# Performance work log

Hardware: AMD Instinct MI355X
Metric: run time of the kernel (lower is better)

The kernel has to match this reference:

```python
import jax, jax.numpy as jnp
import numpy as np

B, D, C, H, L = 32768, 64, 64, 1024, 6
EPS = 1e-5
NIN = (D - D // 2) + C  # unchanged half + cond = 96
SPLIT = D // 2          # 32


def setup_inputs() -> dict:
    key = jax.random.key(0)
    ks = jax.random.split(key, 12)
    s = 0.05
    return {
        "z": jax.random.normal(ks[0], (B, D), jnp.float32),
        "cond": jax.random.normal(ks[1], (B, C), jnp.float32),
        "W1": jax.random.normal(ks[2], (L, NIN, H), jnp.float32) * s,
        "b1": jax.random.normal(ks[3], (L, H), jnp.float32) * s,
        "W2": jax.random.normal(ks[4], (L, H, H), jnp.float32) * s,
        "b2": jax.random.normal(ks[5], (L, H), jnp.float32) * s,
        "Ws": jax.random.normal(ks[6], (L, H, SPLIT), jnp.float32) * s,
        "bs": jax.random.normal(ks[7], (L, SPLIT), jnp.float32) * s,
        "Wt": jax.random.normal(ks[8], (L, H, SPLIT), jnp.float32) * s,
        "bt": jax.random.normal(ks[9], (L, SPLIT), jnp.float32) * s,
        "bn_w": 1.0 + 0.1 * jax.random.normal(ks[10], (L, D), jnp.float32),
        "bn_b": 0.1 * jax.random.normal(ks[11], (L, D), jnp.float32),
    }


def reference(z, cond, W1, b1, W2, b2, Ws, bs, Wt, bt, bn_w, bn_b):
    x = z
    log_det = jnp.zeros((z.shape[0],), z.dtype)
    for i in range(L):
        # 'even' mask keeps even indices on even layers, odd indices otherwise
        if i % 2 == 0:
            keep, chg = np.arange(0, D, 2), np.arange(1, D, 2)
        else:
            keep, chg = np.arange(1, D, 2), np.arange(0, D, 2)
        # 2-layer MLP on [x_keep, cond]
        h = jax.nn.relu(jnp.concatenate([x[:, keep], cond], axis=1) @ W1[i] + b1[i])
        h = jax.nn.relu(h @ W2[i] + b2[i])
        log_s = jnp.tanh(h @ Ws[i] + bs[i])          # (B, SPLIT)
        t = h @ Wt[i] + bt[i]                         # (B, SPLIT)
        x2t = x[:, chg] * jnp.exp(log_s) + t
        x = jnp.zeros_like(x).at[:, keep].set(x[:, keep]).at[:, chg].set(x2t)
        log_det = log_det + log_s.sum(axis=1)
        # BatchNorm1d, training mode: batch mean / biased variance, eps=1e-5
        mean = x.mean(axis=0)
        var = x.var(axis=0)
        x = (x - mean) * jax.lax.rsqrt(var + EPS) * bn_w[i] + bn_b[i]
        log_det = log_det + jnp.log(jnp.abs(bn_w[i])).sum()
    return x, log_det
```

## Files before the change

kernel.cpp:

```cpp
#include <hip/hip_runtime.h>
#include <math.h>

#define BB 32768
#define DD 64
#define CC 64
#define HH 1024
#define LL 6
#define SPLIT 32
#define NIN 96
#define EPSV 1e-5f

typedef short short8 __attribute__((ext_vector_type(8)));
typedef float f32x4 __attribute__((ext_vector_type(4)));
typedef unsigned short u16;

__device__ __forceinline__ u16 f2bf(float f) {
    union { float f; unsigned int u; } c; c.f = f;
    unsigned int u = c.u + 0x7FFFu + ((c.u >> 16) & 1u);
    return (u16)(u >> 16);
}

__device__ __forceinline__ void gl_lds16(const u16* g, u16* l) {
    __builtin_amdgcn_global_load_lds(
        (const __attribute__((address_space(1))) unsigned int*)g,
        (__attribute__((address_space(3))) unsigned int*)l, 16, 0, 0);
}

#define DSR(dst, addr, off) \
    asm volatile("ds_read_b128 %0, %1 offset:" #off : "=&v"(dst) : "v"(addr))

__global__ void transpose_cvt_kernel(const float* __restrict__ src, u16* __restrict__ dst,
                                     int R, int C, int Rpad,
                                     long long sstride, long long dstride)
{
    __shared__ float tile[32][33];
    const float* s = src + (size_t)blockIdx.z * sstride;
    u16* d = dst + (size_t)blockIdx.z * dstride;
    int r0 = blockIdx.x * 32, c0 = blockIdx.y * 32;
    int tc = threadIdx.x & 31, tr = threadIdx.x >> 5;
#pragma unroll
    for (int i = 0; i < 4; ++i) {
        int r = r0 + tr + i * 8;
        tile[tr + i * 8][tc] = (r < R) ? s[(size_t)r * C + c0 + tc] : 0.f;
    }
    __syncthreads();
#pragma unroll
    for (int i = 0; i < 4; ++i) {
        int cc = tr + i * 8;
        d[(size_t)(c0 + cc) * Rpad + r0 + tc] = f2bf(tile[tc][cc]);
    }
}

__global__ __launch_bounds__(256)
void init_ain_cond_kernel(const float* __restrict__ cond, u16* __restrict__ Ain)
{
    int t = blockIdx.x * 256 + threadIdx.x;
    int c = t % 96, r = t / 96;
    Ain[(size_t)r * 128 + 32 + c] = (c < CC) ? f2bf(cond[(size_t)r * CC + c]) : (u16)0;
}

__global__ __launch_bounds__(256)
void build_keep_kernel(const float* __restrict__ x, u16* __restrict__ Ain, int keep_off)
{
    int t = blockIdx.x * 256 + threadIdx.x;
    int c = t & 31, r = t >> 5;
    Ain[(size_t)r * 128 + c] = f2bf(x[(size_t)r * DD + 2 * c + keep_off]);
}

__global__ __launch_bounds__(512, 2)
void gemm_tiled(const u16* __restrict__ A,
                const u16* __restrict__ Bt,
                const float* __restrict__ bias,
                u16* __restrict__ Cc,
                int K)
{
    __shared__ u16 sA[2][32 * 512];
    __shared__ u16 sB[2][32 * 512];

    const int t = threadIdx.x;
    const int w = t >> 6, lane = t & 63;
    const int lane16 = lane & 15, quad = lane >> 4;
    const int wm = w >> 2, wn = w & 3;

    int id = blockIdx.x;
    int nby = gridDim.x >> 2;
    int xcd = id & 7, slot = id >> 3;
    int bx = slot & 3, byq = slot >> 2;
    int by = xcd * (nby >> 3) + byq;
    const int bm = by * 256, bn = bx * 256;

    const int ntile = K >> 6;

    auto stage_half = [&](int kt, int op, int s, int buf) {
        int k0 = kt * 64 + s * 32 + quad * 8;
#pragma unroll
        for (int r = 0; r < 2; ++r) {
            int i = r * 8 + w;
            int e = s * 16 + i;
            if (op == 0) {
                const u16* g = A + (size_t)(bm + i * 16 + lane16) * K + k0;
                gl_lds16(g, &sA[buf][e * 512]);
            } else {
                const u16* g = Bt + (size_t)(bn + i * 16 + lane16) * K + k0;
                gl_lds16(g, &sB[buf][e * 512]);
            }
        }
    };

    f32x4 acc[8][4];
#pragma unroll
    for (int a = 0; a < 8; ++a)
#pragma unroll
        for (int b = 0; b < 4; ++b) acc[a][b] = (f32x4){0.f, 0.f, 0.f, 0.f};

    const unsigned sAb = (unsigned)(size_t)(__attribute__((address_space(3))) u16*)&sA[0][0];
    const unsigned sBb = (unsigned)(size_t)(__attribute__((address_space(3))) u16*)&sB[0][0];
    const unsigned aoff = (unsigned)(wm * 8 * 1024 + lane * 16);
    const unsigned boff = (unsigned)(wn * 4 * 1024 + lane * 16);

    stage_half(0, 0, 0, 0);
    stage_half(0, 1, 0, 0);
    stage_half(0, 0, 1, 0);
    stage_half(0, 1, 1, 0);
    asm volatile("s_waitcnt vmcnt(0)");
    __builtin_amdgcn_s_barrier();

    short8 af[4], ag[4], bf[4], bg[4];
    for (int kt = 0; kt < ntile; ++kt) {
        const unsigned base = (unsigned)((kt & 1) << 15);
        const unsigned aA0 = sAb + base + aoff;
        const unsigned aB0 = sBb + base + boff;
        const unsigned aA1 = aA0 + 16384;
        const unsigned aB1 = aB0 + 16384;
        const int nb = (kt + 1) & 1;
        const bool more = (kt + 1 < ntile);

        DSR(bf[0], aB0, 0); DSR(bf[1], aB0, 1024);
        DSR(bf[2], aB0, 2048); DSR(bf[3], aB0, 3072);
        DSR(af[0], aA0, 0); DSR(af[1], aA0, 1024);
        DSR(af[2], aA0, 2048); DSR(af[3], aA0, 3072);
        if (more) { stage_half(kt + 1, 0, 0, nb); stage_half(kt + 1, 1, 0, nb); }
        DSR(ag[0], aA0, 4096); DSR(ag[1], aA0, 5120);
        DSR(ag[2], aA0, 6144); DSR(ag[3], aA0, 7168);
        asm volatile("s_waitcnt lgkmcnt(4)");
        __builtin_amdgcn_sched_barrier(0);
        __builtin_amdgcn_s_setprio(1);
#pragma unroll
        for (int a = 0; a < 4; ++a)
#pragma unroll
            for (int b = 0; b < 4; ++b)
                acc[a][b] = __builtin_amdgcn_mfma_f32_16x16x32_bf16(af[a], bf[b], acc[a][b], 0, 0, 0);
        __builtin_amdgcn_s_setprio(0);

        if (more) { stage_half(kt + 1, 0, 1, nb); stage_half(kt + 1, 1, 1, nb); }
        DSR(bg[0], aB1, 0); DSR(bg[1], aB1, 1024);
        DSR(bg[2], aB1, 2048); DSR(bg[3], aB1, 3072);
        DSR(af[0], aA1, 0); DSR(af[1], aA1, 1024);
        DSR(af[2], aA1, 2048); DSR(af[3], aA1, 3072);
        asm volatile("s_waitcnt lgkmcnt(8)");
        __builtin_amdgcn_sched_barrier(0);
        __builtin_amdgcn_s_setprio(1);
#pragma unroll
        for (int a = 0; a < 4; ++a)
#pragma unroll
            for (int b = 0; b < 4; ++b)
                acc[4 + a][b] = __builtin_amdgcn_mfma_f32_16x16x32_bf16(ag[a], bf[b], acc[4 + a][b], 0, 0, 0);
        __builtin_amdgcn_s_setprio(0);

        DSR(ag[0], aA1, 4096); DSR(ag[1], aA1, 5120);
        DSR(ag[2], aA1, 6144); DSR(ag[3], aA1, 7168);
        asm volatile("s_waitcnt lgkmcnt(4)");
        __builtin_amdgcn_sched_barrier(0);
        __builtin_amdgcn_s_setprio(1);
#pragma unroll
        for (int a = 0; a < 4; ++a)
#pragma unroll
            for (int b = 0; b < 4; ++b)
                acc[a][b] = __builtin_amdgcn_mfma_f32_16x16x32_bf16(af[a], bg[b], acc[a][b], 0, 0, 0);
        __builtin_amdgcn_s_setprio(0);

        asm volatile("s_waitcnt lgkmcnt(0)");
        __builtin_amdgcn_sched_barrier(0);
        __builtin_amdgcn_s_setprio(1);
#pragma unroll
        for (int a = 0; a < 4; ++a)
#pragma unroll
            for (int b = 0; b < 4; ++b)
                acc[4 + a][b] = __builtin_amdgcn_mfma_f32_16x16x32_bf16(ag[a], bg[b], acc[4 + a][b], 0, 0, 0);
        __builtin_amdgcn_s_setprio(0);

        asm volatile("s_waitcnt vmcnt(0)");
        __builtin_amdgcn_s_barrier();
    }
    __syncthreads();

    constexpr int ES = 72;
    float bv[4];
#pragma unroll
    for (int b = 0; b < 4; ++b) bv[b] = bias[bn + wn * 64 + b * 16 + lane16];
    u16* scr = ((u16*)sB) + w * (16 * ES);
#pragma unroll
    for (int a = 0; a < 8; ++a) {
#pragma unroll
        for (int b = 0; b < 4; ++b)
#pragma unroll
            for (int r = 0; r < 4; ++r) {
                float v = fmaxf(acc[a][b][r] + bv[b], 0.f);
                scr[(quad * 4 + r) * ES + b * 16 + lane16] = f2bf(v);
            }
#pragma unroll
        for (int ch = 0; ch < 2; ++ch) {
            int row = ch * 8 + (lane >> 3), colc = (lane & 7) * 8;
            short8 v = *(const short8*)(scr + row * ES + colc);
            *(short8*)(Cc + (size_t)(bm + wm * 128 + a * 16 + row) * 1024 + bn + wn * 64 + colc) = v;
        }
    }
}

__global__ __launch_bounds__(512, 2)
void gemm1_once(const u16* __restrict__ A,
                const u16* __restrict__ Bt,
                const float* __restrict__ bias,
                u16* __restrict__ Cc)
{
    __shared__ u16 sA[2][32 * 512];
    __shared__ u16 sB[2][32 * 512];

    const int t = threadIdx.x;
    const int w = t >> 6, lane = t & 63;
    const int lane16 = lane & 15, quad = lane >> 4;
    const int wm = w >> 2, wn = w & 3;

    int id = blockIdx.x;
    int nby = gridDim.x >> 2;
    int xcd = id & 7, slot = id >> 3;
    int bx = slot & 3, byq = slot >> 2;
    int by = xcd * (nby >> 3) + byq;
    const int bm = by * 256, bn = bx * 256;

    auto stage_half = [&](int kt, int op, int s, int buf) {
        int k0 = kt * 64 + s * 32 + quad * 8;
#pragma unroll
        for (int r = 0; r < 2; ++r) {
            int i = r * 8 + w;
            int e = s * 16 + i;
            if (op == 0) {
                const u16* g = A + (size_t)(bm + i * 16 + lane16) * 128 + k0;
                gl_lds16(g, &sA[buf][e * 512]);
            } else {
                const u16* g = Bt + (size_t)(bn + i * 16 + lane16) * 128 + k0;
                gl_lds16(g, &sB[buf][e * 512]);
            }
        }
    };

    f32x4 acc[8][4];
#pragma unroll
    for (int a = 0; a < 8; ++a)
#pragma unroll
        for (int b = 0; b < 4; ++b) acc[a][b] = (f32x4){0.f, 0.f, 0.f, 0.f};

    const unsigned sAb = (unsigned)(size_t)(__attribute__((address_space(3))) u16*)&sA[0][0];
    const unsigned sBb = (unsigned)(size_t)(__attribute__((address_space(3))) u16*)&sB[0][0];
    const unsigned aoff = (unsigned)(wm * 8 * 1024 + lane * 16);
    const unsigned boff = (unsigned)(wn * 4 * 1024 + lane * 16);

#pragma unroll
    for (int kt = 0; kt < 2; ++kt) {
        stage_half(kt, 0, 0, kt);
        stage_half(kt, 1, 0, kt);
        stage_half(kt, 0, 1, kt);
        stage_half(kt, 1, 1, kt);
    }
    __syncthreads();

    short8 af[4], ag[4], bf[4], bg[4];
#pragma unroll
    for (int kt = 0; kt < 2; ++kt) {
        const unsigned base = (unsigned)(kt << 15);
        const unsigned aA0 = sAb + base + aoff;
        const unsigned aB0 = sBb + base + boff;
        const unsigned aA1 = aA0 + 16384;
        const unsigned aB1 = aB0 + 16384;

        DSR(bf[0], aB0, 0); DSR(bf[1], aB0, 1024);
        DSR(bf[2], aB0, 2048); DSR(bf[3], aB0, 3072);
        DSR(af[0], aA0, 0); DSR(af[1], aA0, 1024);
        DSR(af[2], aA0, 2048); DSR(af[3], aA0, 3072);
        DSR(ag[0], aA0, 4096); DSR(ag[1], aA0, 5120);
        DSR(ag[2], aA0, 6144); DSR(ag[3], aA0, 7168);
        asm volatile("s_waitcnt lgkmcnt(4)");
        __builtin_amdgcn_sched_barrier(0);
        __builtin_amdgcn_s_setprio(1);
#pragma unroll
        for (int a = 0; a < 4; ++a)
#pragma unroll
            for (int b = 0; b < 4; ++b)
                acc[a][b] = __builtin_amdgcn_mfma_f32_16x16x32_bf16(af[a], bf[b], acc[a][b], 0, 0, 0);
        __builtin_amdgcn_s_setprio(0);

        DSR(bg[0], aB1, 0); DSR(bg[1], aB1, 1024);
        DSR(bg[2], aB1, 2048); DSR(bg[3], aB1, 3072);
        DSR(af[0], aA1, 0); DSR(af[1], aA1, 1024);
        DSR(af[2], aA1, 2048); DSR(af[3], aA1, 3072);
        asm volatile("s_waitcnt lgkmcnt(8)");
        __builtin_amdgcn_sched_barrier(0);
        __builtin_amdgcn_s_setprio(1);
#pragma unroll
        for (int a = 0; a < 4; ++a)
#pragma unroll
            for (int b = 0; b < 4; ++b)
                acc[4 + a][b] = __builtin_amdgcn_mfma_f32_16x16x32_bf16(ag[a], bf[b], acc[4 + a][b], 0, 0, 0);
        __builtin_amdgcn_s_setprio(0);

        DSR(ag[0], aA1, 4096); DSR(ag[1], aA1, 5120);
        DSR(ag[2], aA1, 6144); DSR(ag[3], aA1, 7168);
        asm volatile("s_waitcnt lgkmcnt(4)");
        __builtin_amdgcn_sched_barrier(0);
        __builtin_amdgcn_s_setprio(1);
#pragma unroll
        for (int a = 0; a < 4; ++a)
#pragma unroll
            for (int b = 0; b < 4; ++b)
                acc[a][b] = __builtin_amdgcn_mfma_f32_16x16x32_bf16(af[a], bg[b], acc[a][b], 0, 0, 0);
        __builtin_amdgcn_s_setprio(0);

        asm volatile("s_waitcnt lgkmcnt(0)");
        __builtin_amdgcn_sched_barrier(0);
        __builtin_amdgcn_s_setprio(1);
#pragma unroll
        for (int a = 0; a < 4; ++a)
#pragma unroll
            for (int b = 0; b < 4; ++b)
                acc[4 + a][b] = __builtin_amdgcn_mfma_f32_16x16x32_bf16(ag[a], bg[b], acc[4 + a][b], 0, 0, 0);
        __builtin_amdgcn_s_setprio(0);
    }
    __syncthreads();

    constexpr int ES = 72;
    float bv[4];
#pragma unroll
    for (int b = 0; b < 4; ++b) bv[b] = bias[bn + wn * 64 + b * 16 + lane16];
    u16* scr = ((u16*)sB) + w * (16 * ES);
#pragma unroll
    for (int a = 0; a < 8; ++a) {
#pragma unroll
        for (int b = 0; b < 4; ++b)
#pragma unroll
            for (int r = 0; r < 4; ++r) {
                float v = fmaxf(acc[a][b][r] + bv[b], 0.f);
                scr[(quad * 4 + r) * ES + b * 16 + lane16] = f2bf(v);
            }
#pragma unroll
        for (int ch = 0; ch < 2; ++ch) {
            int row = ch * 8 + (lane >> 3), colc = (lane & 7) * 8;
            short8 v = *(const short8*)(scr + row * ES + colc);
            *(short8*)(Cc + (size_t)(bm + wm * 128 + a * 16 + row) * 1024 + bn + wn * 64 + colc) = v;
        }
    }
}

__global__ __launch_bounds__(512)
void gemm3_coupling(const u16* __restrict__ A,
                    const u16* __restrict__ Bt,
                    const float* __restrict__ bs, const float* __restrict__ bt,
                    float* __restrict__ x, float* __restrict__ log_det,
                    float* __restrict__ stat_sum, float* __restrict__ stat_sumsq,
                    int keep_off, int row0)
{
    constexpr int ST_STRIDE = 66;
    __shared__ u16 sB[128 * 512];
    __shared__ float ssum[8][64], ssum2[8][64];
    float* sst = (float*)sB;

    const int t = threadIdx.x;
    const int w = t >> 6, lane = t & 63;
    const int lane16 = lane & 15, quad = lane >> 4;
    const int bm = blockIdx.x * 128;

#pragma unroll
    for (int r = 0; r < 16; ++r) {
        int e = r * 8 + w;
        int s = e >> 2, j = e & 3;
        const u16* g = Bt + (size_t)(j * 16 + lane16) * HH + s * 32 + quad * 8;
        gl_lds16(g, &sB[e * 512]);
    }

    f32x4 acc[4];
#pragma unroll
    for (int j = 0; j < 4; ++j) acc[j] = (f32x4){0.f, 0.f, 0.f, 0.f};

    const u16* Arow = A + (size_t)(bm + w * 16 + lane16) * HH + quad * 8;

    __syncthreads();

#pragma unroll 4
    for (int s = 0; s < 32; ++s) {
        short8 af = *(const short8*)(Arow + s * 32);
        const u16* bb = sB + s * 2048 + lane * 8;
#pragma unroll
        for (int j = 0; j < 4; ++j) {
            short8 bfr = *(const short8*)(bb + j * 512);
            acc[j] = __builtin_amdgcn_mfma_f32_16x16x32_bf16(af, bfr, acc[j], 0, 0, 0);
        }
    }
    __syncthreads();

#pragma unroll
    for (int j = 0; j < 4; ++j)
#pragma unroll
        for (int r = 0; r < 4; ++r)
            sst[(w * 16 + quad * 4 + r) * ST_STRIDE + j * 16 + lane16] = acc[j][r];
    __syncthreads();

    const int f = lane;
    const bool is_chg = ((f & 1) != keep_off);
    const int j = f >> 1;
    float bsj = 0.f, btj = 0.f;
    if (is_chg) { bsj = bs[j]; btj = bt[j]; }

    float lsum = 0.f, lsum2 = 0.f;
    for (int i = 0; i < 16; ++i) {
        int crow = w * 16 + i;
        int grow = row0 + bm + crow;
        float xv = x[(size_t)grow * DD + f];
        float ld = 0.f;
        if (is_chg) {
            float s_raw = sst[crow * ST_STRIDE + j];
            float t_raw = sst[crow * ST_STRIDE + SPLIT + j];
            float ls = tanhf(s_raw + bsj);
            float tv = t_raw + btj;
            xv = xv * expf(ls) + tv;
            x[(size_t)grow * DD + f] = xv;
            ld = ls;
        }
        for (int off = 32; off > 0; off >>= 1) ld += __shfl_down(ld, off, 64);
        if (f == 0) log_det[grow] += ld;
        lsum  += xv;
        lsum2 += xv * xv;
    }

    ssum[w][f]  = lsum;
    ssum2[w][f] = lsum2;
    __syncthreads();
    if (t < 64) {
        float a = 0.f, b = 0.f;
#pragma unroll
        for (int g = 0; g < 8; ++g) { a += ssum[g][t]; b += ssum2[g][t]; }
        atomicAdd(stat_sum + t, a);
        atomicAdd(stat_sumsq + t, b);
    }
}

__global__ __launch_bounds__(256)
void normalize_kernel(const float* __restrict__ xin, float* __restrict__ xout,
                      const float* __restrict__ stat_sum, const float* __restrict__ stat_sumsq,
                      const float* __restrict__ bn_w, const float* __restrict__ bn_b,
                      float* __restrict__ log_det,
                      u16* __restrict__ Ain, int off_next)
{
    __shared__ float sscale[64], sshift[64], scsum;
    int t = threadIdx.x;
    if (t < 64) {
        const float invB = 1.f / (float)BB;
        float mean = stat_sum[t] * invB;
        float var  = stat_sumsq[t] * invB - mean * mean;
        float inv  = rsqrtf(var + EPSV);
        float wv   = bn_w[t];
        float sc   = inv * wv;
        sscale[t] = sc;
        sshift[t] = bn_b[t] - mean * sc;
        float lg = logf(fabsf(wv));
        for (int off = 32; off > 0; off >>= 1) lg += __shfl_down(lg, off, 64);
        if (t == 0) scsum = lg;
    }
    __syncthreads();

    int idx = blockIdx.x * blockDim.x + t;
    int f0 = (idx & 15) * 4;
    int row = idx >> 4;
    float4 v = ((const float4*)xin)[idx];
    v.x = v.x * sscale[f0 + 0] + sshift[f0 + 0];
    v.y = v.y * sscale[f0 + 1] + sshift[f0 + 1];
    v.z = v.z * sscale[f0 + 2] + sshift[f0 + 2];
    v.w = v.w * sscale[f0 + 3] + sshift[f0 + 3];
    ((float4*)xout)[idx] = v;
    if ((idx & 15) == 0) log_det[row] += scsum;
    if (Ain) {
        float a0 = off_next ? v.y : v.x;
        float a1 = off_next ? v.w : v.z;
        ushort2 u; u.x = f2bf(a0); u.y = f2bf(a1);
        *(ushort2*)(Ain + (size_t)row * 128 + (f0 >> 1)) = u;
    }
}

extern "C" void kernel_launch(void* const* d_in, const int* in_sizes, int n_in,
                              void* d_out, int out_size, void* d_ws, size_t ws_size,
                              hipStream_t stream)
{
    const float* z    = (const float*)d_in[0];
    const float* cond = (const float*)d_in[1];
    const float* W1   = (const float*)d_in[2];
    const float* b1   = (const float*)d_in[3];
    const float* W2   = (const float*)d_in[4];
    const float* b2   = (const float*)d_in[5];
    const float* Ws   = (const float*)d_in[6];
    const float* bs   = (const float*)d_in[7];
    const float* Wt   = (const float*)d_in[8];
    const float* bt   = (const float*)d_in[9];
    const float* bn_w = (const float*)d_in[10];
    const float* bn_b = (const float*)d_in[11];

    float* out_x  = (float*)d_out;
    float* out_ld = out_x + (size_t)BB * DD;

    char* p = (char*)d_ws;
    size_t used = 0;
    auto alloc = [&](size_t bytes) { void* q = p + used; used += (bytes + 255) & ~(size_t)255; return q; };

    float* xbuf = (float*)alloc((size_t)BB * DD * 4);
    u16*   w1t  = (u16*)alloc((size_t)LL * HH * 128 * 2);
    u16*   w2t  = (u16*)alloc((size_t)LL * HH * HH * 2);
    u16*   wstt = (u16*)alloc((size_t)LL * 64 * HH * 2);
    u16*   Ain  = (u16*)alloc((size_t)BB * 128 * 2);
    float* stat_sum   = (float*)alloc(64 * 4);
    float* stat_sumsq = (float*)alloc(64 * 4);

    int CH = BB;
    while (CH > 8192 && used + (size_t)CH * 4096 + 4096 > ws_size) CH >>= 1;
    u16* h1 = (u16*)alloc((size_t)CH * HH * 2);
    u16* h2 = (u16*)alloc((size_t)CH * HH * 2);

    hipMemcpyAsync(xbuf, z, (size_t)BB * DD * sizeof(float), hipMemcpyDeviceToDevice, stream);
    hipMemsetAsync(out_ld, 0, (size_t)BB * sizeof(float), stream);

    transpose_cvt_kernel<<<dim3(128/32, HH/32, LL), 256, 0, stream>>>(
        W1, w1t, NIN, HH, 128, (long long)NIN * HH, (long long)HH * 128);
    transpose_cvt_kernel<<<dim3(HH/32, HH/32, LL), 256, 0, stream>>>(
        W2, w2t, HH, HH, HH, (long long)HH * HH, (long long)HH * HH);
    transpose_cvt_kernel<<<dim3(HH/32, SPLIT/32, LL), 256, 0, stream>>>(
        Ws, wstt, HH, SPLIT, HH, (long long)HH * SPLIT, (long long)64 * HH);
    transpose_cvt_kernel<<<dim3(HH/32, SPLIT/32, LL), 256, 0, stream>>>(
        Wt, wstt + (size_t)SPLIT * HH, HH, SPLIT, HH, (long long)HH * SPLIT, (long long)64 * HH);

    init_ain_cond_kernel<<<BB * 96 / 256, 256, 0, stream>>>(cond, Ain);
    build_keep_kernel<<<BB * 32 / 256, 256, 0, stream>>>(xbuf, Ain, 0);

    for (int l = 0; l < LL; ++l) {
        const int off = l & 1;
        hipMemsetAsync(stat_sum, 0, 2 * 64 * sizeof(float), stream);

        for (int c = 0; c < BB / CH; ++c) {
            const int row0 = c * CH;

            gemm1_once<<<(CH / 256) * 4, 512, 0, stream>>>(
                Ain + (size_t)row0 * 128, w1t + (size_t)l * HH * 128,
                b1 + (size_t)l * HH, h1);

            gemm_tiled<<<(CH / 256) * 4, 512, 0, stream>>>(
                h1, w2t + (size_t)l * HH * HH,
                b2 + (size_t)l * HH, h2, HH);

            gemm3_coupling<<<CH / 128, 512, 0, stream>>>(
                h2, wstt + (size_t)l * 64 * HH,
                bs + (size_t)l * SPLIT, bt + (size_t)l * SPLIT,
                xbuf, out_ld, stat_sum, stat_sumsq, off, row0);
        }

        float* xout = (l == LL - 1) ? out_x : xbuf;
        u16* ain_next = (l < LL - 1) ? Ain : nullptr;
        normalize_kernel<<<(BB * DD / 4) / 256, 256, 0, stream>>>(
            xbuf, xout, stat_sum, stat_sumsq,
            bn_w + (size_t)l * DD, bn_b + (size_t)l * DD,
            out_ld, ain_next, (l + 1) & 1);
    }
}
```

Before: 997.5 us.

## Fuse scale/translate projection into second GEMM epilogue, drop h2 buffer

The second MLP GEMM now multiplies each 256-column slice of its ReLU output by the matching slice of the Ws/Wt weights in its epilogue using MFMA. It writes per-column-block partial s/t sums to a small fp32 buffer instead of materialising the full h2 activation. The coupling kernel then sums the four partials rather than running its own K=1024 GEMM, and the batch chunking is removed. This trades a large bf16 round trip through memory for LDS atomics, extra epilogue work and a partial-sum buffer read.

Result: slower. 1.940 ms (+94.5%).

```diff
diff --git a/kernel.cpp b/kernel.cpp
--- a/kernel.cpp
+++ b/kernel.cpp
@@ -68,14 +68,15 @@
 }
 
 __global__ __launch_bounds__(512, 2)
-void gemm_tiled(const u16* __restrict__ A,
-                const u16* __restrict__ Bt,
-                const float* __restrict__ bias,
-                u16* __restrict__ Cc,
-                int K)
-{
-    __shared__ u16 sA[2][32 * 512];
-    __shared__ u16 sB[2][32 * 512];
+void gemm2_fused(const u16* __restrict__ A,
+                 const u16* __restrict__ Bt,
+                 const float* __restrict__ bias,
+                 const u16* __restrict__ Wst,
+                 float* __restrict__ st_part)
+{
+    __shared__ u16 LDSBUF[65536];
+    const unsigned sAb = (unsigned)(size_t)(__attribute__((address_space(3))) u16*)&LDSBUF[0];
+    const unsigned sBb = sAb + 65536;
 
     const int t = threadIdx.x;
     const int w = t >> 6, lane = t & 63;
@@ -89,8 +90,6 @@
     int by = xcd * (nby >> 3) + byq;
     const int bm = by * 256, bn = bx * 256;
 
-    const int ntile = K >> 6;
-
     auto stage_half = [&](int kt, int op, int s, int buf) {
         int k0 = kt * 64 + s * 32 + quad * 8;
 #pragma unroll
@@ -98,23 +97,31 @@
             int i = r * 8 + w;
             int e = s * 16 + i;
             if (op == 0) {
-                const u16* g = A + (size_t)(bm + i * 16 + lane16) * K + k0;
-                gl_lds16(g, &sA[buf][e * 512]);
+                const u16* g = A + (size_t)(bm + i * 16 + lane16) * 1024 + k0;
+                gl_lds16(g, &LDSBUF[buf * 16384 + e * 512]);
             } else {
-                const u16* g = Bt + (size_t)(bn + i * 16 + lane16) * K + k0;
-                gl_lds16(g, &sB[buf][e * 512]);
+                const u16* g = Bt + (size_t)(bn + i * 16 + lane16) * 1024 + k0;
+                gl_lds16(g, &LDSBUF[32768 + buf * 16384 + e * 512]);
             }
         }
     };
 
+    auto stage_W = [&]() {
+#pragma unroll
+        for (int r = 0; r < 4; ++r) {
+            int e = r * 8 + w;
+            int s = e >> 2, jg = e & 3;
+            const u16* g = Wst + (size_t)(jg * 16 + lane16) * HH + bn + s * 32 + quad * 8;
+            gl_lds16(g, &LDSBUF[e * 512]);
+        }
+    };
+
     f32x4 acc[8][4];
 #pragma unroll
     for (int a = 0; a < 8; ++a)
 #pragma unroll
         for (int b = 0; b < 4; ++b) acc[a][b] = (f32x4){0.f, 0.f, 0.f, 0.f};
 
-    const unsigned sAb = (unsigned)(size_t)(__attribute__((address_space(3))) u16*)&sA[0][0];
-    const unsigned sBb = (unsigned)(size_t)(__attribute__((address_space(3))) u16*)&sB[0][0];
     const unsigned aoff = (unsigned)(wm * 8 * 1024 + lane * 16);
     const unsigned boff = (unsigned)(wn * 4 * 1024 + lane * 16);
 
@@ -126,20 +133,21 @@
     __builtin_amdgcn_s_barrier();
 
     short8 af[4], ag[4], bf[4], bg[4];
-    for (int kt = 0; kt < ntile; ++kt) {
+    for (int kt = 0; kt < 16; ++kt) {
         const unsigned base = (unsigned)((kt & 1) << 15);
         const unsigned aA0 = sAb + base + aoff;
         const unsigned aB0 = sBb + base + boff;
         const unsigned aA1 = aA0 + 16384;
         const unsigned aB1 = aB0 + 16384;
         const int nb = (kt + 1) & 1;
-        const bool more = (kt + 1 < ntile);
+        const bool more = (kt + 1 < 16);
 
         DSR(bf[0], aB0, 0); DSR(bf[1], aB0, 1024);
         DSR(bf[2], aB0, 2048); DSR(bf[3], aB0, 3072);
         DSR(af[0], aA0, 0); DSR(af[1], aA0, 1024);
         DSR(af[2], aA0, 2048); DSR(af[3], aA0, 3072);
         if (more) { stage_half(kt + 1, 0, 0, nb); stage_half(kt + 1, 1, 0, nb); }
+        else      { stage_W(); }
         DSR(ag[0], aA0, 4096); DSR(ag[1], aA0, 5120);
         DSR(ag[2], aA0, 6144); DSR(ag[3], aA0, 7168);
         asm volatile("s_waitcnt lgkmcnt(4)");
@@ -194,26 +202,58 @@
     }
     __syncthreads();
 
+    constexpr int STB = 72;
+    float* stb = (float*)(LDSBUF + 16384);
+    for (int i = t; i < 256 * STB; i += 512) stb[i] = 0.f;
+    __syncthreads();
+
+    short8 wb[2][4];
+#pragma unroll
+    for (int ks = 0; ks < 2; ++ks)
+#pragma unroll
+        for (int jg = 0; jg < 4; ++jg)
+            wb[ks][jg] = *(const short8*)(LDSBUF + (size_t)(((wn * 2 + ks) * 4 + jg) * 512 + lane * 8));
+
     constexpr int ES = 72;
     float bv[4];
 #pragma unroll
     for (int b = 0; b < 4; ++b) bv[b] = bias[bn + wn * 64 + b * 16 + lane16];
-    u16* scr = ((u16*)sB) + w * (16 * ES);
-#pragma unroll
-    for (int a = 0; a < 8; ++a) {
+    u16* scr = LDSBUF + 53248 + w * 1152;
+
+#pragma unroll
+    for (int m = 0; m < 8; ++m) {
 #pragma unroll
         for (int b = 0; b < 4; ++b)
 #pragma unroll
             for (int r = 0; r < 4; ++r) {
-                float v = fmaxf(acc[a][b][r] + bv[b], 0.f);
+                float v = fmaxf(acc[m][b][r] + bv[b], 0.f);
                 scr[(quad * 4 + r) * ES + b * 16 + lane16] = f2bf(v);
             }
-#pragma unroll
-        for (int ch = 0; ch < 2; ++ch) {
-            int row = ch * 8 + (lane >> 3), colc = (lane & 7) * 8;
-            short8 v = *(const short8*)(scr + row * ES + colc);
-            *(short8*)(Cc + (size_t)(bm + wm * 128 + a * 16 + row) * 1024 + bn + wn * 64 + colc) = v;
+        short8 a0 = *(const short8*)(scr + lane16 * ES + quad * 8);
+        short8 a1 = *(const short8*)(scr + lane16 * ES + 32 + quad * 8);
+        f32x4 stacc[4];
+#pragma unroll
+        for (int jt = 0; jt < 4; ++jt) stacc[jt] = (f32x4){0.f, 0.f, 0.f, 0.f};
+#pragma unroll
+        for (int jt = 0; jt < 4; ++jt) {
+            stacc[jt] = __builtin_amdgcn_mfma_f32_16x16x32_bf16(a0, wb[0][jt], stacc[jt], 0, 0, 0);
+            stacc[jt] = __builtin_amdgcn_mfma_f32_16x16x32_bf16(a1, wb[1][jt], stacc[jt], 0, 0, 0);
         }
+        int rowbase = wm * 128 + m * 16 + quad * 4;
+#pragma unroll
+        for (int jt = 0; jt < 4; ++jt)
+#pragma unroll
+            for (int r = 0; r < 4; ++r)
+                atomicAdd(&stb[(rowbase + r) * STB + jt * 16 + lane16], stacc[jt][r]);
+    }
+    __syncthreads();
+
+    float* dst = st_part + ((size_t)bx * BB + bm) * 64;
+#pragma unroll
+    for (int r8 = 0; r8 < 8; ++r8) {
+        int row = r8 * 32 + (t >> 4), c4 = (t & 15) * 4;
+        f32x4 v = *(const f32x4*)(stb + row * STB + c4);
+        *(f32x4*)(dst + (size_t)row * 64 + c4) = v;
     }
 }
 
@@ -361,57 +401,16 @@
 }
 
 __global__ __launch_bounds__(512)
-void gemm3_coupling(const u16* __restrict__ A,
-                    const u16* __restrict__ Bt,
-                    const float* __restrict__ bs, const float* __restrict__ bt,
-                    float* __restrict__ x, float* __restrict__ log_det,
-                    float* __restrict__ stat_sum, float* __restrict__ stat_sumsq,
-                    int keep_off, int row0)
-{
-    constexpr int ST_STRIDE = 66;
-    __shared__ u16 sB[128 * 512];
+void coupling_kernel(const float* __restrict__ st_part,
+                     const float* __restrict__ bs, const float* __restrict__ bt,
+                     float* __restrict__ x, float* __restrict__ log_det,
+                     float* __restrict__ stat_sum, float* __restrict__ stat_sumsq,
+                     int keep_off)
+{
     __shared__ float ssum[8][64], ssum2[8][64];
-    float* sst = (float*)sB;
-
     const int t = threadIdx.x;
     const int w = t >> 6, lane = t & 63;
-    const int lane16 = lane & 15, quad = lane >> 4;
     const int bm = blockIdx.x * 128;
-
-#pragma unroll
-    for (int r = 0; r < 16; ++r) {
-        int e = r * 8 + w;
-        int s = e >> 2, j = e & 3;
-        const u16* g = Bt + (size_t)(j * 16 + lane16) * HH + s * 32 + quad * 8;
-        gl_lds16(g, &sB[e * 512]);
-    }
-
-    f32x4 acc[4];
-#pragma unroll
-    for (int j = 0; j < 4; ++j) acc[j] = (f32x4){0.f, 0.f, 0.f, 0.f};
-
-    const u16* Arow = A + (size_t)(bm + w * 16 + lane16) * HH + quad * 8;
-
-    __syncthreads();
-
-#pragma unroll 4
-    for (int s = 0; s < 32; ++s) {
-        short8 af = *(const short8*)(Arow + s * 32);
-        const u16* bb = sB + s * 2048 + lane * 8;
-#pragma unroll
-        for (int j = 0; j < 4; ++j) {
-            short8 bfr = *(const short8*)(bb + j * 512);
-            acc[j] = __builtin_amdgcn_mfma_f32_16x16x32_bf16(af, bfr, acc[j], 0, 0, 0);
-        }
-    }
-    __syncthreads();
-
-#pragma unroll
-    for (int j = 0; j < 4; ++j)
-#pragma unroll
-        for (int r = 0; r < 4; ++r)
-            sst[(w * 16 + quad * 4 + r) * ST_STRIDE + j * 16 + lane16] = acc[j][r];
-    __syncthreads();
 
     const int f = lane;
     const bool is_chg = ((f & 1) != keep_off);
@@ -421,13 +420,17 @@
 
     float lsum = 0.f, lsum2 = 0.f;
     for (int i = 0; i < 16; ++i) {
-        int crow = w * 16 + i;
-        int grow = row0 + bm + crow;
+        int grow = bm + w * 16 + i;
         float xv = x[(size_t)grow * DD + f];
         float ld = 0.f;
         if (is_chg) {
-            float s_raw = sst[crow * ST_STRIDE + j];
-            float t_raw = sst[crow * ST_STRIDE + SPLIT + j];
+            float s_raw = 0.f, t_raw = 0.f;
+#pragma unroll
+            for (int p = 0; p < 4; ++p) {
+                const float* q = st_part + ((size_t)p * BB + grow) * 64;
+                s_raw += q[j];
+                t_raw += q[32 + j];
+            }
             float ls = tanhf(s_raw + bsj);
             float tv = t_raw + btj;
             xv = xv * expf(ls) + tv;
@@ -525,11 +528,8 @@
     u16*   Ain  = (u16*)alloc((size_t)BB * 128 * 2);
     float* stat_sum   = (float*)alloc(64 * 4);
     float* stat_sumsq = (float*)alloc(64 * 4);
-
-    int CH = BB;
-    while (CH > 8192 && used + (size_t)CH * 4096 + 4096 > ws_size) CH >>= 1;
-    u16* h1 = (u16*)alloc((size_t)CH * HH * 2);
-    u16* h2 = (u16*)alloc((size_t)CH * HH * 2);
+    u16*   h1   = (u16*)alloc((size_t)BB * HH * 2);
+    float* st_part = (float*)alloc((size_t)4 * BB * 64 * 4);
 
     hipMemcpyAsync(xbuf, z, (size_t)BB * DD * sizeof(float), hipMemcpyDeviceToDevice, stream);
     hipMemsetAsync(out_ld, 0, (size_t)BB * sizeof(float), stream);
@@ -550,22 +550,16 @@
         const int off = l & 1;
         hipMemsetAsync(stat_sum, 0, 2 * 64 * sizeof(float), stream);
 
-        for (int c = 0; c < BB / CH; ++c) {
-            const int row0 = c * CH;
-
-            gemm1_once<<<(CH / 256) * 4, 512, 0, stream>>>(
-                Ain + (size_t)row0 * 128, w1t + (size_t)l * HH * 128,
-                b1 + (size_t)l * HH, h1);
-
-            gemm_tiled<<<(CH / 256) * 4, 512, 0, stream>>>(
-                h1, w2t + (size_t)l * HH * HH,
-                b2 + (size_t)l * HH, h2, HH);
-
-            gemm3_coupling<<<CH / 128, 512, 0, stream>>>(
-                h2, wstt + (size_t)l * 64 * HH,
-                bs + (size_t)l * SPLIT, bt + (size_t)l * SPLIT,
-                xbuf, out_ld, stat_sum, stat_sumsq, off, row0);
-        }
+        gemm1_once<<<(BB / 256) * 4, 512, 0, stream>>>(
+            Ain, w1t + (size_t)l * HH * 128, b1 + (size_t)l * HH, h1);
+
+        gemm2_fused<<<(BB / 256) * 4, 512, 0, stream>>>(
+            h1, w2t + (size_t)l * HH * HH, b2 + (size_t)l * HH,
+            wstt + (size_t)l * 64 * HH, st_part);
+
+        coupling_kernel<<<BB / 128, 512, 0, stream>>>(
+            st_part, bs + (size_t)l * SPLIT, bt + (size_t)l * SPLIT,
+            xbuf, out_ld, stat_sum, stat_sumsq, off);
 
         float* xout = (l == LL - 1) ? out_x : xbuf;
         u16* ain_next = (l < LL - 1) ? Ain : nullptr;
```

## Use triple-buffered 32-wide K tiles with two-stage-ahead global-to-LDS prefetch

Applied to the files above, without the earlier changes.

Reworks the main GEMM loop from double-buffered 64-wide K tiles to triple-buffered 32-wide K tiles. Global-to-LDS loads are issued two tiles ahead, and the wait before each barrier allows the next tile's loads to stay in flight (vmcnt(4)). The goal is to hide global memory latency better without increasing LDS use. In exchange there are twice as many barriers per K, less MFMA work between syncs, and the ring-buffer vmcnt accounting has to stay correct.

Measured after the change: 932.1 us. 1.07x faster.

```diff
diff --git a/kernel.cpp b/kernel.cpp
--- a/kernel.cpp
+++ b/kernel.cpp
@@ -74,8 +74,8 @@
                 u16* __restrict__ Cc,
                 int K)
 {
-    __shared__ u16 sA[2][32 * 512];
-    __shared__ u16 sB[2][32 * 512];
+    __shared__ u16 sA[3][16 * 512];
+    __shared__ u16 sB[3][16 * 512];
 
     const int t = threadIdx.x;
     const int w = t >> 6, lane = t & 63;
@@ -89,20 +89,20 @@
     int by = xcd * (nby >> 3) + byq;
     const int bm = by * 256, bn = bx * 256;
 
-    const int ntile = K >> 6;
-
-    auto stage_half = [&](int kt, int op, int s, int buf) {
-        int k0 = kt * 64 + s * 32 + quad * 8;
-#pragma unroll
-        for (int r = 0; r < 2; ++r) {
-            int i = r * 8 + w;
-            int e = s * 16 + i;
-            if (op == 0) {
-                const u16* g = A + (size_t)(bm + i * 16 + lane16) * K + k0;
+    const int ntile = K >> 5;
+
+    auto stage = [&](int kt, int buf) {
+        int k0 = kt * 32 + quad * 8;
+#pragma unroll
+        for (int p = 0; p < 4; ++p) {
+            int e = p * 8 + w;
+            if (e < 16) {
+                const u16* g = A + (size_t)(bm + e * 16 + lane16) * K + k0;
                 gl_lds16(g, &sA[buf][e * 512]);
             } else {
-                const u16* g = Bt + (size_t)(bn + i * 16 + lane16) * K + k0;
-                gl_lds16(g, &sB[buf][e * 512]);
+                int j = e - 16;
+                const u16* g = Bt + (size_t)(bn + j * 16 + lane16) * K + k0;
+                gl_lds16(g, &sB[buf][j * 512]);
             }
         }
     };
@@ -118,30 +118,26 @@
     const unsigned aoff = (unsigned)(wm * 8 * 1024 + lane * 16);
     const unsigned boff = (unsigned)(wn * 4 * 1024 + lane * 16);
 
-    stage_half(0, 0, 0, 0);
-    stage_half(0, 1, 0, 0);
-    stage_half(0, 0, 1, 0);
-    stage_half(0, 1, 1, 0);
-    asm volatile("s_waitcnt vmcnt(0)");
+    stage(0, 0);
+    stage(1, 1);
+    asm volatile("s_waitcnt vmcnt(4)");
     __builtin_amdgcn_s_barrier();
 
-    short8 af[4], ag[4], bf[4], bg[4];
+    int cb = 0;
     for (int kt = 0; kt < ntile; ++kt) {
-        const unsigned base = (unsigned)((kt & 1) << 15);
-        const unsigned aA0 = sAb + base + aoff;
-        const unsigned aB0 = sBb + base + boff;
-        const unsigned aA1 = aA0 + 16384;
-        const unsigned aB1 = aB0 + 16384;
-        const int nb = (kt + 1) & 1;
-        const bool more = (kt + 1 < ntile);
-
-        DSR(bf[0], aB0, 0); DSR(bf[1], aB0, 1024);
-        DSR(bf[2], aB0, 2048); DSR(bf[3], aB0, 3072);
-        DSR(af[0], aA0, 0); DSR(af[1], aA0, 1024);
-        DSR(af[2], aA0, 2048); DSR(af[3], aA0, 3072);
-        if (more) { stage_half(kt + 1, 0, 0, nb); stage_half(kt + 1, 1, 0, nb); }
-        DSR(ag[0], aA0, 4096); DSR(ag[1], aA0, 5120);
-        DSR(ag[2], aA0, 6144); DSR(ag[3], aA0, 7168);
+        const unsigned aA = sAb + (unsigned)(cb * 16384) + aoff;
+        const unsigned aB = sBb + (unsigned)(cb * 16384) + boff;
+        int sb = cb - 1; if (sb < 0) sb = 2;
+
+        short8 af[4], ag[4], bf[4];
+        DSR(bf[0], aB, 0);    DSR(bf[1], aB, 1024);
+        DSR(bf[2], aB, 2048); DSR(bf[3], aB, 3072);
+        DSR(af[0], aA, 0);    DSR(af[1], aA, 1024);
+        DSR(af[2], aA, 2048); DSR(af[3], aA, 3072);
+        if (kt + 2 < ntile) stage(kt + 2, sb);
+        DSR(ag[0], aA, 4096); DSR(ag[1], aA, 5120);
+        DSR(ag[2], aA, 6144); DSR(ag[3], aA, 7168);
+
         asm volatile("s_waitcnt lgkmcnt(4)");
         __builtin_amdgcn_sched_barrier(0);
         __builtin_amdgcn_s_setprio(1);
@@ -152,12 +148,7 @@
                 acc[a][b] = __builtin_amdgcn_mfma_f32_16x16x32_bf16(af[a], bf[b], acc[a][b], 0, 0, 0);
         __builtin_amdgcn_s_setprio(0);
 
-        if (more) { stage_half(kt + 1, 0, 1, nb); stage_half(kt + 1, 1, 1, nb); }
-        DSR(bg[0], aB1, 0); DSR(bg[1], aB1, 1024);
-        DSR(bg[2], aB1, 2048); DSR(bg[3], aB1, 3072);
-        DSR(af[0], aA1, 0); DSR(af[1], aA1, 1024);
-        DSR(af[2], aA1, 2048); DSR(af[3], aA1, 3072);
-        asm volatile("s_waitcnt lgkmcnt(8)");
+        asm volatile("s_waitcnt lgkmcnt(0)");
         __builtin_amdgcn_sched_barrier(0);
         __builtin_amdgcn_s_setprio(1);
 #pragma unroll
@@ -167,30 +158,11 @@
                 acc[4 + a][b] = __builtin_amdgcn_mfma_f32_16x16x32_bf16(ag[a], bf[b], acc[4 + a][b], 0, 0, 0);
         __builtin_amdgcn_s_setprio(0);
 
-        DSR(ag[0], aA1, 4096); DSR(ag[1], aA1, 5120);
-        DSR(ag[2], aA1, 6144); DSR(ag[3], aA1, 7168);
-        asm volatile("s_waitcnt lgkmcnt(4)");
-        __builtin_amdgcn_sched_barrier(0);
-        __builtin_amdgcn_s_setprio(1);
-#pragma unroll
-        for (int a = 0; a < 4; ++a)
-#pragma unroll
-            for (int b = 0; b < 4; ++b)
-                acc[a][b] = __builtin_amdgcn_mfma_f32_16x16x32_bf16(af[a], bg[b], acc[a][b], 0, 0, 0);
-        __builtin_amdgcn_s_setprio(0);
-
-        asm volatile("s_waitcnt lgkmcnt(0)");
-        __builtin_amdgcn_sched_barrier(0);
-        __builtin_amdgcn_s_setprio(1);
-#pragma unroll
-        for (int a = 0; a < 4; ++a)
-#pragma unroll
-            for (int b = 0; b < 4; ++b)
-                acc[4 + a][b] = __builtin_amdgcn_mfma_f32_16x16x32_bf16(ag[a], bg[b], acc[4 + a][b], 0, 0, 0);
-        __builtin_amdgcn_s_setprio(0);
-
-        asm volatile("s_waitcnt vmcnt(0)");
+        if (kt + 2 < ntile) asm volatile("s_waitcnt vmcnt(4)");
+        else                asm volatile("s_waitcnt vmcnt(0)");
         __builtin_amdgcn_s_barrier();
+
+        cb = (cb == 2) ? 0 : cb + 1;
     }
     __syncthreads();
 
```
